# Kernel tuning notes

Measured on AMD Instinct MI355X. Metric: run time of the kernel, lower is better.

The kernel has to match this reference:

```python
import jax, jax.numpy as jnp
import numpy as np

B, C, S = 32, 2048, 28   # batch, in_channels, spatial_size
M, Q = 4, 1              # number of RAEs, hidden units per RAE
LAMBDA = 1e-3            # ridge regularization for the ELM-style decoder solve
EPS = 1e-10              # lp_norm_layer eps


def setup_inputs() -> dict:
    key = jax.random.key(0)
    k1, k2 = jax.random.split(key)
    x = jax.random.normal(k1, (B, C, S, S), dtype=jnp.float32)
    # Random (seeded, untrained) encoder weights for the M randomized autoencoders.
    W = jax.random.normal(k2, (M, C, Q), dtype=jnp.float32)
    return {"x": x, "W": W}


def _pos_encoding(n, d, dtype):
    # Standard sinusoidal 1D positional encoding over the n=H*W pixel positions,
    # d = channel dim (RADAM adds it to the per-pixel feature vectors).
    pos = jnp.arange(n, dtype=dtype)[:, None]                 # (n, 1)
    i = jnp.arange(0, d, 2, dtype=dtype)                      # (d/2,)
    div = jnp.exp(-(i / d) * jnp.log(jnp.asarray(10000.0, dtype)))
    pe = jnp.zeros((n, d), dtype)
    pe = pe.at[:, 0::2].set(jnp.sin(pos * div))
    pe = pe.at[:, 1::2].set(jnp.cos(pos * div))
    return pe


def reference(x, W):
    # x: (B, C, H, W) feature maps; W: (M, C, Q) random encoder weights.
    b, c, h, w = x.shape
    n = h * w
    # lp_norm_layer: L2-normalize each channel's spatial map jointly over (H, W).
    norm = jnp.sqrt(jnp.sum(x * x, axis=(2, 3), keepdims=True))
    xn = x / jnp.maximum(norm, EPS)
    # Resize(spatial_size) is identity (input already at spatial_size); flatten.
    feats = xn.reshape(b, c, n).transpose(0, 2, 1)            # (B, N, C) pixels-as-samples
    pe = _pos_encoding(n, c, x.dtype)                         # (N, C)
    xp = feats + pe[None]                                     # pos-encoded input
    # Hidden activations of all M RAEs for all batch elements at once.
    hid = jax.nn.sigmoid(jnp.einsum('bnc,mcq->bmnq', xp, W))  # (B, M, N, Q)
    # Closed-form ridge (ELM) decoder: beta = (H^T H + lam I)^{-1} H^T X
    hth = jnp.einsum('bmnq,bmnp->bmqp', hid, hid)             # (B, M, Q, Q)
    htx = jnp.einsum('bmnq,bnc->bmqc', hid, xp)               # (B, M, Q, C)
    eye = LAMBDA * jnp.eye(Q, dtype=x.dtype)
    beta = jnp.linalg.solve(hth + eye, htx)                   # (B, M, Q, C)
    # Sum decoder weights over the M RAEs (the per-rae pooled += in the loop).
    pooled = jnp.nan_to_num(jnp.sum(beta, axis=1))            # (B, Q, C)
    return pooled
```

## Files before the change

### kernel.cpp

```cpp
#include <hip/hip_runtime.h>
#include <math.h>

#define BB 32
#define CC 2048
#define NN 784
#define NF4 196
#define MM 4
#define LAMBDA_ 1e-3f
#define EPS_ 1e-10f
#define LOG1E4 9.210340371976184f
#define NORM_BLOCKS (BB * CC / 4)

__device__ __forceinline__ float wred(float v) {
#pragma unroll
  for (int off = 32; off > 0; off >>= 1) v += __shfl_down(v, off, 64);
  return v;
}

__global__ __launch_bounds__(256) void k_norm_pew(const float* __restrict__ x,
                                                  const float* __restrict__ W,
                                                  float* __restrict__ inv_norm,
                                                  float* __restrict__ peW) {
  int bid  = blockIdx.x;
  int lane = threadIdx.x & 63;
  if (bid < NORM_BLOCKS) {
    int idx = bid * 4 + (threadIdx.x >> 6);
    const float4* row = (const float4*)(x + (size_t)idx * NN);
    float ss = 0.f;
    for (int f = lane; f < NF4; f += 64) {
      float4 v = row[f];
      ss += v.x * v.x + v.y * v.y + v.z * v.z + v.w * v.w;
    }
    ss = wred(ss);
    if (lane == 0) inv_norm[idx] = 1.f / fmaxf(sqrtf(ss), EPS_);
  } else {
    int n = bid - NORM_BLOCKS;
    int m = threadIdx.x >> 6;
    float acc = 0.f;
    for (int c = lane; c < CC; c += 64) {
      float di  = expf(-((float)(c & ~1) / (float)CC) * LOG1E4);
      float arg = (float)n * di;
      float pe  = (c & 1) ? cosf(arg) : sinf(arg);
      acc += pe * W[m * CC + c];
    }
    acc = wred(acc);
    if (lane == 0) peW[m * NN + n] = acc;
  }
}

template <int NCH>
__global__ __launch_bounds__(256) void k_sacc(const float* __restrict__ x,
                                              const float* __restrict__ W,
                                              const float* __restrict__ inv_norm,
                                              float4* __restrict__ sPart4) {
  int t  = threadIdx.x;
  int ch = blockIdx.x;
  int b  = blockIdx.y;
  if (t >= NF4) return;
  const float4* xb  = (const float4*)(x + (size_t)b * CC * NN);
  const float* invb = inv_norm + b * CC;
  float4 a0 = {0,0,0,0}, a1 = {0,0,0,0}, a2 = {0,0,0,0}, a3 = {0,0,0,0};
  const int cper = CC / NCH;
  int c0 = ch * cper;
#pragma unroll 4
  for (int i = 0; i < cper; ++i) {
    int c = c0 + i;
    float4 xv = xb[(size_t)c * NF4 + t];
    float iw = invb[c];
    float w0 = iw * W[0 * CC + c];
    float w1 = iw * W[1 * CC + c];
    float w2 = iw * W[2 * CC + c];
    float w3 = iw * W[3 * CC + c];
    a0.x += xv.x * w0; a0.y += xv.y * w0; a0.z += xv.z * w0; a0.w += xv.w * w0;
    a1.x += xv.x * w1; a1.y += xv.y * w1; a1.z += xv.z * w1; a1.w += xv.w * w1;
    a2.x += xv.x * w2; a2.y += xv.y * w2; a2.z += xv.z * w2; a2.w += xv.w * w2;
    a3.x += xv.x * w3; a3.y += xv.y * w3; a3.z += xv.z * w3; a3.w += xv.w * w3;
  }
  size_t base = (((size_t)b * NCH + ch) * MM) * NF4 + t;
  sPart4[base + 0 * NF4] = a0;
  sPart4[base + 1 * NF4] = a1;
  sPart4[base + 2 * NF4] = a2;
  sPart4[base + 3 * NF4] = a3;
}

template <int NCH>
__global__ __launch_bounds__(256) void k_hid(const float* __restrict__ sPart,
                                             const float* __restrict__ peW,
                                             float* __restrict__ hid4) {
  int n = blockIdx.x * 256 + threadIdx.x;
  int b = blockIdx.y;
  if (n >= NN) return;
  float h[MM];
#pragma unroll
  for (int m = 0; m < MM; ++m) {
    float s = peW[m * NN + n];
#pragma unroll
    for (int ch = 0; ch < NCH; ++ch)
      s += sPart[(((size_t)b * NCH + ch) * MM + m) * NN + n];
    h[m] = 1.f / (1.f + __expf(-s));
  }
  float4 hv = make_float4(h[0], h[1], h[2], h[3]);
  *(float4*)(hid4 + ((size_t)b * NN + n) * 4) = hv;
}

__global__ __launch_bounds__(256) void k_out(const float* __restrict__ x,
                                             const float* __restrict__ hid4,
                                             const float* __restrict__ inv_norm,
                                             float* __restrict__ out) {
  int idx  = blockIdx.x * 4 + (threadIdx.x >> 6);
  int lane = threadIdx.x & 63;
  int b = idx >> 11;
  int c = idx & (CC - 1);
  const float4* row = (const float4*)(x + (size_t)idx * NN);
  const float4* hb  = (const float4*)(hid4 + (size_t)b * NN * 4);
  float di = __expf(-((float)(c & ~1) * (1.0f / CC)) * LOG1E4);
  bool use_sin = !(c & 1);
  float aX0=0,aX1=0,aX2=0,aX3=0, aP0=0,aP1=0,aP2=0,aP3=0, aD0=0,aD1=0,aD2=0,aD3=0;
  for (int f = lane; f < NF4; f += 64) {
    float4 xv = row[f];
    int n = f * 4;
    float4 h0 = hb[n + 0], h1 = hb[n + 1], h2 = hb[n + 2], h3 = hb[n + 3];
    float a0 = (float)(n + 0) * di, a1 = (float)(n + 1) * di;
    float a2 = (float)(n + 2) * di, a3 = (float)(n + 3) * di;
    float p0 = use_sin ? __sinf(a0) : __cosf(a0);
    float p1 = use_sin ? __sinf(a1) : __cosf(a1);
    float p2 = use_sin ? __sinf(a2) : __cosf(a2);
    float p3 = use_sin ? __sinf(a3) : __cosf(a3);
    aX0 += xv.x*h0.x + xv.y*h1.x + xv.z*h2.x + xv.w*h3.x;
    aX1 += xv.x*h0.y + xv.y*h1.y + xv.z*h2.y + xv.w*h3.y;
    aX2 += xv.x*h0.z + xv.y*h1.z + xv.z*h2.z + xv.w*h3.z;
    aX3 += xv.x*h0.w + xv.y*h1.w + xv.z*h2.w + xv.w*h3.w;
    aP0 += p0*h0.x + p1*h1.x + p2*h2.x + p3*h3.x;
    aP1 += p0*h0.y + p1*h1.y + p2*h2.y + p3*h3.y;
    aP2 += p0*h0.z + p1*h1.z + p2*h2.z + p3*h3.z;
    aP3 += p0*h0.w + p1*h1.w + p2*h2.w + p3*h3.w;
    aD0 += h0.x*h0.x + h1.x*h1.x + h2.x*h2.x + h3.x*h3.x;
    aD1 += h0.y*h0.y + h1.y*h1.y + h2.y*h2.y + h3.y*h3.y;
    aD2 += h0.z*h0.z + h1.z*h1.z + h2.z*h2.z + h3.z*h3.z;
    aD3 += h0.w*h0.w + h1.w*h1.w + h2.w*h2.w + h3.w*h3.w;
  }
  aX0 = wred(aX0); aX1 = wred(aX1); aX2 = wred(aX2); aX3 = wred(aX3);
  aP0 = wred(aP0); aP1 = wred(aP1); aP2 = wred(aP2); aP3 = wred(aP3);
  aD0 = wred(aD0); aD1 = wred(aD1); aD2 = wred(aD2); aD3 = wred(aD3);
  if (lane == 0) {
    float inv = inv_norm[idx];
    float r = (inv * aX0 + aP0) / (aD0 + LAMBDA_)
            + (inv * aX1 + aP1) / (aD1 + LAMBDA_)
            + (inv * aX2 + aP2) / (aD2 + LAMBDA_)
            + (inv * aX3 + aP3) / (aD3 + LAMBDA_);
    if (isnan(r)) r = 0.f;
    else if (isinf(r)) r = (r > 0.f) ? 3.4028234663852886e38f : -3.4028234663852886e38f;
    out[idx] = r;
  }
}

extern "C" void kernel_launch(void* const* d_in, const int* in_sizes, int n_in,
                              void* d_out, int out_size, void* d_ws, size_t ws_size,
                              hipStream_t stream) {
  const float* x = (const float*)d_in[0];
  const float* W = (const float*)d_in[1];
  float* out = (float*)d_out;
  float* ws  = (float*)d_ws;

  float* inv_norm = ws;
  float* peW      = inv_norm + (size_t)BB * CC;
  float* hid4     = peW + (size_t)MM * NN;
  float* sPart    = hid4 + (size_t)BB * NN * MM;

  const size_t base_floats = (size_t)BB * CC + MM * NN + (size_t)BB * NN * MM;
  const size_t need16 = (base_floats + (size_t)BB * 16 * MM * NN) * sizeof(float);

  k_norm_pew<<<NORM_BLOCKS + NN, 256, 0, stream>>>(x, W, inv_norm, peW);
  if (ws_size >= need16) {
    k_sacc<16><<<dim3(16, BB), 256, 0, stream>>>(x, W, inv_norm, (float4*)sPart);
    k_hid<16><<<dim3((NN + 255) / 256, BB), 256, 0, stream>>>(sPart, peW, hid4);
  } else {
    k_sacc<8><<<dim3(8, BB), 256, 0, stream>>>(x, W, inv_norm, (float4*)sPart);
    k_hid<8><<<dim3((NN + 255) / 256, BB), 256, 0, stream>>>(sPart, peW, hid4);
  }
  k_out<<<NORM_BLOCKS, 256, 0, stream>>>(x, hid4, inv_norm, out);
}
```

Baseline: 149.8 us.

## Fuse channel-norm and positional-W projection into the partial-sum kernel

Removes the separate norm/peW kernel. The channel L2 norm is now computed inside the partial-sum kernel from x tiles already loaded in registers, via block-level reduction over TILE channels. The peW projection runs in extra blocks of the same grid, and the channel split grows to 32 when workspace allows. This drops one full pass over x and one launch, but adds two __syncthreads per tile of 8 channels and idles 60 of 256 threads.

Result: slower. 210.5 us (+40.5%).

```diff
diff --git a/kernel.cpp b/kernel.cpp
--- a/kernel.cpp
+++ b/kernel.cpp
@@ -6,6 +6,7 @@
 #define NN 784
 #define NF4 196
 #define MM 4
+#define TILE 8
 #define LAMBDA_ 1e-3f
 #define EPS_ 1e-10f
 #define LOG1E4 9.210340371976184f
@@ -17,70 +18,93 @@
   return v;
 }
 
-__global__ __launch_bounds__(256) void k_norm_pew(const float* __restrict__ x,
-                                                  const float* __restrict__ W,
-                                                  float* __restrict__ inv_norm,
-                                                  float* __restrict__ peW) {
-  int bid  = blockIdx.x;
-  int lane = threadIdx.x & 63;
-  if (bid < NORM_BLOCKS) {
-    int idx = bid * 4 + (threadIdx.x >> 6);
-    const float4* row = (const float4*)(x + (size_t)idx * NN);
-    float ss = 0.f;
-    for (int f = lane; f < NF4; f += 64) {
-      float4 v = row[f];
-      ss += v.x * v.x + v.y * v.y + v.z * v.z + v.w * v.w;
-    }
-    ss = wred(ss);
-    if (lane == 0) inv_norm[idx] = 1.f / fmaxf(sqrtf(ss), EPS_);
-  } else {
-    int n = bid - NORM_BLOCKS;
-    int m = threadIdx.x >> 6;
-    float acc = 0.f;
-    for (int c = lane; c < CC; c += 64) {
-      float di  = expf(-((float)(c & ~1) / (float)CC) * LOG1E4);
-      float arg = (float)n * di;
-      float pe  = (c & 1) ? cosf(arg) : sinf(arg);
-      acc += pe * W[m * CC + c];
-    }
-    acc = wred(acc);
-    if (lane == 0) peW[m * NN + n] = acc;
-  }
-}
-
 template <int NCH>
-__global__ __launch_bounds__(256) void k_sacc(const float* __restrict__ x,
-                                              const float* __restrict__ W,
-                                              const float* __restrict__ inv_norm,
-                                              float4* __restrict__ sPart4) {
-  int t  = threadIdx.x;
+__global__ __launch_bounds__(256) void k_sacc_fused(const float* __restrict__ x,
+                                                    const float* __restrict__ W,
+                                                    float* __restrict__ inv_norm,
+                                                    float* __restrict__ peW,
+                                                    float4* __restrict__ sPart4) {
   int ch = blockIdx.x;
   int b  = blockIdx.y;
-  if (t >= NF4) return;
-  const float4* xb  = (const float4*)(x + (size_t)b * CC * NN);
-  const float* invb = inv_norm + b * CC;
-  float4 a0 = {0,0,0,0}, a1 = {0,0,0,0}, a2 = {0,0,0,0}, a3 = {0,0,0,0};
+  int t  = threadIdx.x;
+  int lane = t & 63;
+  int wv   = t >> 6;
+
+  if (ch == NCH) {
+    const int NPS = (NN + BB - 1) / BB;
+    int n0 = b * NPS, n1 = (n0 + NPS < NN) ? n0 + NPS : NN;
+    int m = wv;
+    for (int n = n0; n < n1; ++n) {
+      float acc = 0.f;
+      for (int c = lane; c < CC; c += 64) {
+        float di  = __expf(-((float)(c & ~1) * (1.f / CC)) * LOG1E4);
+        float arg = (float)n * di;
+        float pe  = (c & 1) ? __cosf(arg) : __sinf(arg);
+        acc += pe * W[m * CC + c];
+      }
+      acc = wred(acc);
+      if (lane == 0) peW[m * NN + n] = acc;
+    }
+    return;
+  }
+
   const int cper = CC / NCH;
+  bool valid = t < NF4;
+  int tt = valid ? t : 0;
+  const float4* xb = (const float4*)(x + (size_t)b * CC * NN);
+
+  __shared__ float red[4][TILE];
+  __shared__ float inv_s[TILE];
+
+  float4 a0{0,0,0,0}, a1{0,0,0,0}, a2{0,0,0,0}, a3{0,0,0,0};
   int c0 = ch * cper;
-#pragma unroll 4
-  for (int i = 0; i < cper; ++i) {
-    int c = c0 + i;
-    float4 xv = xb[(size_t)c * NF4 + t];
-    float iw = invb[c];
-    float w0 = iw * W[0 * CC + c];
-    float w1 = iw * W[1 * CC + c];
-    float w2 = iw * W[2 * CC + c];
-    float w3 = iw * W[3 * CC + c];
-    a0.x += xv.x * w0; a0.y += xv.y * w0; a0.z += xv.z * w0; a0.w += xv.w * w0;
-    a1.x += xv.x * w1; a1.y += xv.y * w1; a1.z += xv.z * w1; a1.w += xv.w * w1;
-    a2.x += xv.x * w2; a2.y += xv.y * w2; a2.z += xv.z * w2; a2.w += xv.w * w2;
-    a3.x += xv.x * w3; a3.y += xv.y * w3; a3.z += xv.z * w3; a3.w += xv.w * w3;
-  }
-  size_t base = (((size_t)b * NCH + ch) * MM) * NF4 + t;
-  sPart4[base + 0 * NF4] = a0;
-  sPart4[base + 1 * NF4] = a1;
-  sPart4[base + 2 * NF4] = a2;
-  sPart4[base + 3 * NF4] = a3;
+
+  for (int tile = 0; tile < cper / TILE; ++tile) {
+    int cb = c0 + tile * TILE;
+    float4 xv[TILE];
+    float sq[TILE];
+#pragma unroll
+    for (int i = 0; i < TILE; ++i) {
+      float4 v = xb[(size_t)(cb + i) * NF4 + tt];
+      if (!valid) { v.x = 0.f; v.y = 0.f; v.z = 0.f; v.w = 0.f; }
+      xv[i] = v;
+      sq[i] = v.x * v.x + v.y * v.y + v.z * v.z + v.w * v.w;
+    }
+#pragma unroll
+    for (int i = 0; i < TILE; ++i) sq[i] = wred(sq[i]);
+    if (lane == 0) {
+#pragma unroll
+      for (int i = 0; i < TILE; ++i) red[wv][i] = sq[i];
+    }
+    __syncthreads();
+    if (t < TILE) {
+      float s = red[0][t] + red[1][t] + red[2][t] + red[3][t];
+      float inv = 1.f / fmaxf(sqrtf(s), EPS_);
+      inv_s[t] = inv;
+      inv_norm[b * CC + cb + t] = inv;
+    }
+    __syncthreads();
+#pragma unroll
+    for (int i = 0; i < TILE; ++i) {
+      int c = cb + i;
+      float iw = inv_s[i];
+      float w0 = iw * W[0 * CC + c];
+      float w1 = iw * W[1 * CC + c];
+      float w2 = iw * W[2 * CC + c];
+      float w3 = iw * W[3 * CC + c];
+      a0.x += xv[i].x * w0; a0.y += xv[i].y * w0; a0.z += xv[i].z * w0; a0.w += xv[i].w * w0;
+      a1.x += xv[i].x * w1; a1.y += xv[i].y * w1; a1.z += xv[i].z * w1; a1.w += xv[i].w * w1;
+      a2.x += xv[i].x * w2; a2.y += xv[i].y * w2; a2.z += xv[i].z * w2; a2.w += xv[i].w * w2;
+      a3.x += xv[i].x * w3; a3.y += xv[i].y * w3; a3.z += xv[i].z * w3; a3.w += xv[i].w * w3;
+    }
+  }
+  if (valid) {
+    size_t base = (((size_t)b * NCH + ch) * MM) * NF4 + t;
+    sPart4[base + 0 * NF4] = a0;
+    sPart4[base + 1 * NF4] = a1;
+    sPart4[base + 2 * NF4] = a2;
+    sPart4[base + 3 * NF4] = a3;
+  }
 }
 
 template <int NCH>
@@ -168,15 +192,18 @@
   float* sPart    = hid4 + (size_t)BB * NN * MM;
 
   const size_t base_floats = (size_t)BB * CC + MM * NN + (size_t)BB * NN * MM;
+  const size_t need32 = (base_floats + (size_t)BB * 32 * MM * NN) * sizeof(float);
   const size_t need16 = (base_floats + (size_t)BB * 16 * MM * NN) * sizeof(float);
 
-  k_norm_pew<<<NORM_BLOCKS + NN, 256, 0, stream>>>(x, W, inv_norm, peW);
-  if (ws_size >= need16) {
-    k_sacc<16><<<dim3(16, BB), 256, 0, stream>>>(x, W, inv_norm, (float4*)sPart);
-    k_hid<16><<<dim3((NN + 255) / 256, BB), 256, 0, stream>>>(sPart, peW, hid4);
+  if (ws_size >= need32) {
+    k_sacc_fused<32><<<dim3(33, BB), 256, 0, stream>>>(x, W, inv_norm, peW, (float4*)sPart);
+    k_hid<32><<<dim3(4, BB), 256, 0, stream>>>(sPart, peW, hid4);
+  } else if (ws_size >= need16) {
+    k_sacc_fused<16><<<dim3(17, BB), 256, 0, stream>>>(x, W, inv_norm, peW, (float4*)sPart);
+    k_hid<16><<<dim3(4, BB), 256, 0, stream>>>(sPart, peW, hid4);
   } else {
-    k_sacc<8><<<dim3(8, BB), 256, 0, stream>>>(x, W, inv_norm, (float4*)sPart);
-    k_hid<8><<<dim3((NN + 255) / 256, BB), 256, 0, stream>>>(sPart, peW, hid4);
+    k_sacc_fused<8><<<dim3(9, BB), 256, 0, stream>>>(x, W, inv_norm, peW, (float4*)sPart);
+    k_hid<8><<<dim3(4, BB), 256, 0, stream>>>(sPart, peW, hid4);
   }
   k_out<<<NORM_BLOCKS, 256, 0, stream>>>(x, hid4, inv_norm, out);
 }
```

## Fuse channel L2 norm into projection accumulation with per-wave register double-buffering

Applied to the files above, without the earlier changes.

Removes the separate read of x that only computed per-channel norms. Each wave now loads a whole channel row into registers, computes its norm by cross-lane reduction, and applies it immediately in the projection accumulation, writing inv_norm as a side output. Loads are double-buffered across channels, and the channel split grows to 64 or 32 partial chunks, which gives more parallelism but more partial-sum traffic in k_hid. The positional-encoding projection moves to its own kernel using fast transcendental intrinsics, a small accuracy risk.

After: 133.7 us. 10.8% less time.

```diff
diff --git a/kernel.cpp b/kernel.cpp
--- a/kernel.cpp
+++ b/kernel.cpp
@@ -17,70 +17,91 @@
   return v;
 }
 
-__global__ __launch_bounds__(256) void k_norm_pew(const float* __restrict__ x,
-                                                  const float* __restrict__ W,
-                                                  float* __restrict__ inv_norm,
-                                                  float* __restrict__ peW) {
-  int bid  = blockIdx.x;
+__global__ __launch_bounds__(256) void k_peW(const float* __restrict__ W,
+                                             float* __restrict__ peW) {
+  int n    = blockIdx.x;
+  int m    = threadIdx.x >> 6;
   int lane = threadIdx.x & 63;
-  if (bid < NORM_BLOCKS) {
-    int idx = bid * 4 + (threadIdx.x >> 6);
-    const float4* row = (const float4*)(x + (size_t)idx * NN);
-    float ss = 0.f;
-    for (int f = lane; f < NF4; f += 64) {
-      float4 v = row[f];
-      ss += v.x * v.x + v.y * v.y + v.z * v.z + v.w * v.w;
+  float acc = 0.f;
+  for (int c = lane; c < CC; c += 64) {
+    float di  = __expf(-((float)(c & ~1) * (1.f / CC)) * LOG1E4);
+    float arg = (float)n * di;
+    float pe  = (c & 1) ? __cosf(arg) : __sinf(arg);
+    acc += pe * W[m * CC + c];
+  }
+  acc = wred(acc);
+  if (lane == 0) peW[m * NN + n] = acc;
+}
+
+template <int NCH>
+__global__ __launch_bounds__(256) void k_sacc2(const float* __restrict__ x,
+                                               const float* __restrict__ W,
+                                               float* __restrict__ inv_norm,
+                                               float4* __restrict__ sPart4) {
+  constexpr int CPER = CC / NCH;
+  int b    = blockIdx.y;
+  int wv   = threadIdx.x >> 6;
+  int lane = threadIdx.x & 63;
+  int ch   = blockIdx.x * 4 + wv;
+  int c0   = ch * CPER;
+  const float4* xb = (const float4*)(x + ((size_t)b * CC + c0) * NN);
+  const float4 z = make_float4(0.f, 0.f, 0.f, 0.f);
+
+  float4 acc[MM][4];
+#pragma unroll
+  for (int m = 0; m < MM; ++m)
+#pragma unroll
+    for (int j = 0; j < 4; ++j) acc[m][j] = z;
+
+  float4 xA[4], xB[4];
+
+  auto LOAD = [&](float4* dst, int i) {
+    const float4* p = xb + (size_t)i * NF4 + lane;
+    dst[0] = p[0];
+    dst[1] = p[64];
+    dst[2] = p[128];
+    dst[3] = (lane < (NF4 - 192)) ? p[192] : z;
+  };
+  auto COMP = [&](const float4* v, int i) {
+    int c = c0 + i;
+    float sq = v[0].x * v[0].x + v[0].y * v[0].y + v[0].z * v[0].z + v[0].w * v[0].w
+             + v[1].x * v[1].x + v[1].y * v[1].y + v[1].z * v[1].z + v[1].w * v[1].w
+             + v[2].x * v[2].x + v[2].y * v[2].y + v[2].z * v[2].z + v[2].w * v[2].w
+             + v[3].x * v[3].x + v[3].y * v[3].y + v[3].z * v[3].z + v[3].w * v[3].w;
+#pragma unroll
+    for (int o = 1; o < 64; o <<= 1) sq += __shfl_xor(sq, o, 64);
+    float inv = 1.f / fmaxf(sqrtf(sq), EPS_);
+    if (lane == 0) inv_norm[b * CC + c] = inv;
+    float w0 = inv * W[0 * CC + c];
+    float w1 = inv * W[1 * CC + c];
+    float w2 = inv * W[2 * CC + c];
+    float w3 = inv * W[3 * CC + c];
+#pragma unroll
+    for (int j = 0; j < 4; ++j) {
+      float4 v4 = v[j];
+      acc[0][j].x += v4.x * w0; acc[0][j].y += v4.y * w0; acc[0][j].z += v4.z * w0; acc[0][j].w += v4.w * w0;
+      acc[1][j].x += v4.x * w1; acc[1][j].y += v4.y * w1; acc[1][j].z += v4.z * w1; acc[1][j].w += v4.w * w1;
+      acc[2][j].x += v4.x * w2; acc[2][j].y += v4.y * w2; acc[2][j].z += v4.z * w2; acc[2][j].w += v4.w * w2;
+      acc[3][j].x += v4.x * w3; acc[3][j].y += v4.y * w3; acc[3][j].z += v4.z * w3; acc[3][j].w += v4.w * w3;
     }
-    ss = wred(ss);
-    if (lane == 0) inv_norm[idx] = 1.f / fmaxf(sqrtf(ss), EPS_);
-  } else {
-    int n = bid - NORM_BLOCKS;
-    int m = threadIdx.x >> 6;
-    float acc = 0.f;
-    for (int c = lane; c < CC; c += 64) {
-      float di  = expf(-((float)(c & ~1) / (float)CC) * LOG1E4);
-      float arg = (float)n * di;
-      float pe  = (c & 1) ? cosf(arg) : sinf(arg);
-      acc += pe * W[m * CC + c];
+  };
+
+  LOAD(xA, 0);
+  for (int i = 0; i < CPER; i += 2) {
+    LOAD(xB, i + 1);
+    COMP(xA, i);
+    LOAD(xA, (i + 2) & (CPER - 1));
+    COMP(xB, i + 1);
+  }
+
+  size_t base = (((size_t)b * NCH + ch) * MM) * NF4;
+#pragma unroll
+  for (int m = 0; m < MM; ++m)
+#pragma unroll
+    for (int j = 0; j < 4; ++j) {
+      int f = lane + 64 * j;
+      if (f < NF4) sPart4[base + (size_t)m * NF4 + f] = acc[m][j];
     }
-    acc = wred(acc);
-    if (lane == 0) peW[m * NN + n] = acc;
-  }
-}
-
-template <int NCH>
-__global__ __launch_bounds__(256) void k_sacc(const float* __restrict__ x,
-                                              const float* __restrict__ W,
-                                              const float* __restrict__ inv_norm,
-                                              float4* __restrict__ sPart4) {
-  int t  = threadIdx.x;
-  int ch = blockIdx.x;
-  int b  = blockIdx.y;
-  if (t >= NF4) return;
-  const float4* xb  = (const float4*)(x + (size_t)b * CC * NN);
-  const float* invb = inv_norm + b * CC;
-  float4 a0 = {0,0,0,0}, a1 = {0,0,0,0}, a2 = {0,0,0,0}, a3 = {0,0,0,0};
-  const int cper = CC / NCH;
-  int c0 = ch * cper;
-#pragma unroll 4
-  for (int i = 0; i < cper; ++i) {
-    int c = c0 + i;
-    float4 xv = xb[(size_t)c * NF4 + t];
-    float iw = invb[c];
-    float w0 = iw * W[0 * CC + c];
-    float w1 = iw * W[1 * CC + c];
-    float w2 = iw * W[2 * CC + c];
-    float w3 = iw * W[3 * CC + c];
-    a0.x += xv.x * w0; a0.y += xv.y * w0; a0.z += xv.z * w0; a0.w += xv.w * w0;
-    a1.x += xv.x * w1; a1.y += xv.y * w1; a1.z += xv.z * w1; a1.w += xv.w * w1;
-    a2.x += xv.x * w2; a2.y += xv.y * w2; a2.z += xv.z * w2; a2.w += xv.w * w2;
-    a3.x += xv.x * w3; a3.y += xv.y * w3; a3.z += xv.z * w3; a3.w += xv.w * w3;
-  }
-  size_t base = (((size_t)b * NCH + ch) * MM) * NF4 + t;
-  sPart4[base + 0 * NF4] = a0;
-  sPart4[base + 1 * NF4] = a1;
-  sPart4[base + 2 * NF4] = a2;
-  sPart4[base + 3 * NF4] = a3;
 }
 
 template <int NCH>
@@ -94,7 +115,7 @@
 #pragma unroll
   for (int m = 0; m < MM; ++m) {
     float s = peW[m * NN + n];
-#pragma unroll
+#pragma unroll 8
     for (int ch = 0; ch < NCH; ++ch)
       s += sPart[(((size_t)b * NCH + ch) * MM + m) * NN + n];
     h[m] = 1.f / (1.f + __expf(-s));
@@ -168,15 +189,19 @@
   float* sPart    = hid4 + (size_t)BB * NN * MM;
 
   const size_t base_floats = (size_t)BB * CC + MM * NN + (size_t)BB * NN * MM;
-  const size_t need16 = (base_floats + (size_t)BB * 16 * MM * NN) * sizeof(float);
-
-  k_norm_pew<<<NORM_BLOCKS + NN, 256, 0, stream>>>(x, W, inv_norm, peW);
-  if (ws_size >= need16) {
-    k_sacc<16><<<dim3(16, BB), 256, 0, stream>>>(x, W, inv_norm, (float4*)sPart);
-    k_hid<16><<<dim3((NN + 255) / 256, BB), 256, 0, stream>>>(sPart, peW, hid4);
+  const size_t need64 = (base_floats + (size_t)BB * 64 * MM * NN) * sizeof(float);
+  const size_t need32 = (base_floats + (size_t)BB * 32 * MM * NN) * sizeof(float);
+
+  k_peW<<<NN, 256, 0, stream>>>(W, peW);
+  if (ws_size >= need64) {
+    k_sacc2<64><<<dim3(16, BB), 256, 0, stream>>>(x, W, inv_norm, (float4*)sPart);
+    k_hid<64><<<dim3(4, BB), 256, 0, stream>>>(sPart, peW, hid4);
+  } else if (ws_size >= need32) {
+    k_sacc2<32><<<dim3(8, BB), 256, 0, stream>>>(x, W, inv_norm, (float4*)sPart);
+    k_hid<32><<<dim3(4, BB), 256, 0, stream>>>(sPart, peW, hid4);
   } else {
-    k_sacc<8><<<dim3(8, BB), 256, 0, stream>>>(x, W, inv_norm, (float4*)sPart);
-    k_hid<8><<<dim3((NN + 255) / 256, BB), 256, 0, stream>>>(sPart, peW, hid4);
+    k_sacc2<16><<<dim3(4, BB), 256, 0, stream>>>(x, W, inv_norm, (float4*)sPart);
+    k_hid<16><<<dim3(4, BB), 256, 0, stream>>>(sPart, peW, hid4);
   }
   k_out<<<NORM_BLOCKS, 256, 0, stream>>>(x, hid4, inv_norm, out);
 }
```
